# Performance work log

Hardware: AMD Instinct MI355X
Metric: run time of the kernel (lower is better)

The kernel has to match this reference:

```python
import jax, jax.numpy as jnp
import numpy as np

N = 50000
E = 800000
IN_C = 128
HID_C = 128
OUT_C = 128
N_CLS = 40


def setup_inputs() -> dict:
    key = jax.random.key(0)
    ks = jax.random.split(key, 12)
    x = jax.random.normal(ks[0], (N, IN_C), dtype=jnp.float32)
    edge_index = jax.random.randint(ks[1], (2, E), 0, N, dtype=jnp.int64)
    s = 1.0 / np.sqrt(IN_C)
    W_l1 = jax.random.uniform(ks[2], (IN_C, HID_C), jnp.float32, -s, s)
    W_r1 = jax.random.uniform(ks[3], (IN_C, HID_C), jnp.float32, -s, s)
    b1 = jax.random.uniform(ks[4], (HID_C,), jnp.float32, -s, s)
    s2 = 1.0 / np.sqrt(HID_C)
    W_l2 = jax.random.uniform(ks[5], (HID_C, OUT_C), jnp.float32, -s2, s2)
    W_r2 = jax.random.uniform(ks[6], (HID_C, OUT_C), jnp.float32, -s2, s2)
    b2 = jax.random.uniform(ks[7], (OUT_C,), jnp.float32, -s2, s2)
    s3 = 1.0 / np.sqrt(OUT_C)
    W_c = jax.random.uniform(ks[8], (OUT_C, N_CLS), jnp.float32, -s3, s3)
    b_c = jax.random.uniform(ks[9], (N_CLS,), jnp.float32, -s3, s3)
    return {"x": x, "edge_index": edge_index, "W_l1": W_l1, "W_r1": W_r1,
            "b1": b1, "W_l2": W_l2, "W_r2": W_r2, "b2": b2,
            "W_c": W_c, "b_c": b_c}


def _mean_aggregate(x, src, dst, deg_inv):
    # gather source node features over edges, scatter-mean to dst nodes
    msg = x[src]  # [E, C]
    agg = jax.ops.segment_sum(msg, dst, num_segments=N)  # [N, C]
    return agg * deg_inv[:, None]


def _sage_conv(x, src, dst, deg_inv, W_l, W_r, b):
    # PyG SAGEConv (mean aggr): out = agg @ W_l + x @ W_r + b
    agg = _mean_aggregate(x, src, dst, deg_inv)
    return agg @ W_l + x @ W_r + b


def reference(x, edge_index, W_l1, W_r1, b1, W_l2, W_r2, b2, W_c, b_c):
    src, dst = edge_index[0], edge_index[1]
    deg = jax.ops.segment_sum(jnp.ones((E,), jnp.float32), dst, num_segments=N)
    deg_inv = jnp.where(deg > 0, 1.0 / jnp.maximum(deg, 1.0), 0.0)
    h = jax.nn.relu(_sage_conv(x, src, dst, deg_inv, W_l1, W_r1, b1))
    h = jax.nn.relu(_sage_conv(h, src, dst, deg_inv, W_l2, W_r2, b2))
    return h @ W_c + b_c
```

## Files before the change

kernel.cpp:

```cpp
#include <hip/hip_runtime.h>

#define N_NODES 50000
#define N_EDGES 800000
#define C 128
#define NCLS 40
#define KB 98
#define BCAP 9216

typedef short bf16x8 __attribute__((ext_vector_type(8)));
typedef float f32x4 __attribute__((ext_vector_type(4)));
typedef unsigned short ushort_t;

__device__ __forceinline__ unsigned short f32_to_bf16(float f) {
    union { float f; unsigned u; } c; c.f = f;
    unsigned r = (c.u + 0x7FFFu + ((c.u >> 16) & 1u)) >> 16;
    return (unsigned short)r;
}
__device__ __forceinline__ float bf_lo(unsigned u) {
    union { unsigned u; float f; } c; c.u = u << 16; return c.f;
}
__device__ __forceinline__ float bf_hi(unsigned u) {
    union { unsigned u; float f; } c; c.u = u & 0xffff0000u; return c.f;
}
__device__ __forceinline__ unsigned pack_bf16(float lo, float hi) {
    return (unsigned)f32_to_bf16(lo) | ((unsigned)f32_to_bf16(hi) << 16);
}

__global__ __launch_bounds__(256)
void convert_all(const float* __restrict__ Wl1, const float* __restrict__ Wr1,
                 const float* __restrict__ Wl2, const float* __restrict__ Wr2,
                 const float* __restrict__ Wc,  const float* __restrict__ x,
                 ushort_t* __restrict__ Wbf1, ushort_t* __restrict__ Wbf2,
                 ushort_t* __restrict__ Wcb,  ushort_t* __restrict__ xb) {
    int b = blockIdx.x;
    int tid = threadIdx.x;
    if (b < 256) {
        const float* Wl = (b < 128) ? Wl1 : Wl2;
        const float* Wr = (b < 128) ? Wr1 : Wr2;
        ushort_t* Bpre  = (b < 128) ? Wbf1 : Wbf2;
        int idx = (b & 127) * 256 + tid;
        int n = idx >> 8;
        int k = idx & 255;
        float v = (k < 128) ? Wl[k * 128 + n] : Wr[(k - 128) * 128 + n];
        Bpre[n * 256 + k] = f32_to_bf16(v);
    } else if (b < 280) {
        int idx = (b - 256) * 256 + tid;
        if (idx < 48 * 128) {
            int n = idx >> 7;
            int k = idx & 127;
            float v = (n < NCLS) ? Wc[k * NCLS + n] : 0.f;
            Wcb[idx] = f32_to_bf16(v);
        }
    } else {
        int idx = (b - 280) * 256 + tid;
        const float4 v0 = *(const float4*)&x[idx * 8];
        const float4 v1 = *(const float4*)&x[idx * 8 + 4];
        uint4 o;
        o.x = pack_bf16(v0.x, v0.y);
        o.y = pack_bf16(v0.z, v0.w);
        o.z = pack_bf16(v1.x, v1.y);
        o.w = pack_bf16(v1.z, v1.w);
        ((uint4*)xb)[idx] = o;
    }
}

__global__ __launch_bounds__(256)
void bin_kernel(const int* __restrict__ src, const int* __restrict__ dst,
                int* __restrict__ bucket_cnt, unsigned* __restrict__ bucket_data) {
    __shared__ int lh[KB];
    int tid = threadIdx.x;
    int e0 = blockIdx.x * 4096;
    if (tid < KB) lh[tid] = 0;
    __syncthreads();
#pragma unroll
    for (int j = 0; j < 16; ++j) {
        int e = e0 + j * 256 + tid;
        if (e < N_EDGES) atomicAdd(&lh[dst[e] >> 9], 1);
    }
    __syncthreads();
    if (tid < KB) lh[tid] = atomicAdd(&bucket_cnt[tid], lh[tid]);
    __syncthreads();
#pragma unroll
    for (int j = 0; j < 16; ++j) {
        int e = e0 + j * 256 + tid;
        if (e < N_EDGES) {
            int d = dst[e];
            int b = d >> 9;
            int pos = atomicAdd(&lh[b], 1);
            if (pos < BCAP)
                bucket_data[b * BCAP + pos] = (unsigned)src[e] | ((unsigned)(d & 511) << 16);
        }
    }
}

__global__ __launch_bounds__(256)
void build_kernel(const int* __restrict__ bucket_cnt, const unsigned* __restrict__ bucket_data,
                  int* __restrict__ row_ptr, ushort_t* __restrict__ csr16,
                  int* __restrict__ perm) {
    __shared__ int wt[4];
    __shared__ int wt2[4];
    __shared__ int sbases[128];
    __shared__ int hist[512];
    __shared__ int loff[512];
    __shared__ int dhist[64];
    __shared__ ushort_t lcsr[BCAP];
    int tid = threadIdx.x;
    int b = blockIdx.x;
    int n0 = b << 9;
    int nb = min(512, N_NODES - n0);

    int v = 0, x = 0;
    if (tid < 128) {
        v = (tid < KB) ? bucket_cnt[tid] : 0;
        x = v;
#pragma unroll
        for (int off = 1; off < 64; off <<= 1) {
            int t = __shfl_up(x, off, 64);
            if ((tid & 63) >= off) x += t;
        }
        if ((tid & 63) == 63) wt[tid >> 6] = x;
    }
    hist[tid] = 0; hist[tid + 256] = 0;
    __syncthreads();
    if (tid < 128) sbases[tid] = x - v + ((tid >= 64) ? wt[0] : 0);
    __syncthreads();
    int base = sbases[b];
    int ecnt = min(bucket_cnt[b], BCAP);

    for (int i = tid; i < ecnt; i += 256)
        atomicAdd(&hist[bucket_data[b * BCAP + i] >> 16], 1);
    __syncthreads();

    int h0 = hist[2 * tid], h1 = hist[2 * tid + 1];
    int s = h0 + h1;
    int y = s;
#pragma unroll
    for (int off = 1; off < 64; off <<= 1) {
        int t = __shfl_up(y, off, 64);
        if ((tid & 63) >= off) y += t;
    }
    if ((tid & 63) == 63) wt2[tid >> 6] = y;
    __syncthreads();
    int add = 0;
    for (int j = 0; j < (tid >> 6); ++j) add += wt2[j];
    int ex = y + add - s;
    loff[2 * tid] = ex;
    loff[2 * tid + 1] = ex + h0;
    __syncthreads();

    for (int n = tid; n < nb; n += 256) row_ptr[n0 + n] = base + loff[n];
    if (b == KB - 1 && tid == 0) row_ptr[N_NODES] = N_EDGES;
    __syncthreads();

    for (int i = tid; i < ecnt; i += 256) {
        unsigned e = bucket_data[b * BCAP + i];
        int pos = atomicAdd(&loff[e >> 16], 1);
        lcsr[pos] = (ushort_t)(e & 0xFFFFu);
    }
    __syncthreads();
    for (int i = tid; i < ecnt; i += 256) csr16[base + i] = lcsr[i];

    if (tid < 64) dhist[tid] = 0;
    for (int p = tid; p < 512; p += 256) perm[(b << 9) + p] = -1;
    __syncthreads();
    int na = 2 * tid, nbb = 2 * tid + 1;
    int c0 = min(h0, 63), c1 = min(h1, 63);
    if (na < nb)  atomicAdd(&dhist[c0], 1);
    if (nbb < nb) atomicAdd(&dhist[c1], 1);
    __syncthreads();
    if (tid < 64) {
        int v2 = dhist[tid];
        int xs = v2;
#pragma unroll
        for (int off = 1; off < 64; off <<= 1) {
            int t = __shfl_up(xs, off, 64);
            if (tid >= off) xs += t;
        }
        dhist[tid] = xs - v2;
    }
    __syncthreads();
    if (na < nb)  { int pos = atomicAdd(&dhist[c0], 1); perm[(b << 9) + pos] = n0 + na; }
    if (nbb < nb) { int pos = atomicAdd(&dhist[c1], 1); perm[(b << 9) + pos] = n0 + nbb; }
}

__global__ __launch_bounds__(256)
void gather_kernel(const ushort_t* __restrict__ feat,
                   const int* __restrict__ row_ptr,
                   const ushort_t* __restrict__ csr16,
                   const int* __restrict__ perm,
                   ushort_t* __restrict__ agg) {
    const int tid = threadIdx.x;
    const int q = tid & 15;
    const int g = tid >> 4;
    int slot = blockIdx.x * 16 + g;
    int node = perm[slot];
    if (node < 0) return;
    int beg = row_ptr[node], end = row_ptr[node + 1];
    int deg = end - beg;
    const uint4* fb = (const uint4*)feat;

    float a0[8], a1[8], a2[8], a3[8];
#pragma unroll
    for (int j = 0; j < 8; ++j) { a0[j] = 0.f; a1[j] = 0.f; a2[j] = 0.f; a3[j] = 0.f; }

    int nquad = deg >> 2;
    int sx0 = 0, sx1 = 0, sx2 = 0, sx3 = 0;
    if (nquad > 0) {
        sx0 = csr16[beg]; sx1 = csr16[beg + 1]; sx2 = csr16[beg + 2]; sx3 = csr16[beg + 3];
    }
    for (int qd = 0; qd < nquad; ++qd) {
        int s0 = sx0, s1 = sx1, s2 = sx2, s3 = sx3;
        uint4 v0 = fb[s0 * 16 + q];
        uint4 v1 = fb[s1 * 16 + q];
        uint4 v2 = fb[s2 * 16 + q];
        uint4 v3 = fb[s3 * 16 + q];
        if (qd + 1 < nquad) {
            int bs = beg + (qd + 1) * 4;
            sx0 = csr16[bs]; sx1 = csr16[bs + 1]; sx2 = csr16[bs + 2]; sx3 = csr16[bs + 3];
        }
        a0[0] += bf_lo(v0.x); a0[1] += bf_hi(v0.x); a0[2] += bf_lo(v0.y); a0[3] += bf_hi(v0.y);
        a0[4] += bf_lo(v0.z); a0[5] += bf_hi(v0.z); a0[6] += bf_lo(v0.w); a0[7] += bf_hi(v0.w);
        a1[0] += bf_lo(v1.x); a1[1] += bf_hi(v1.x); a1[2] += bf_lo(v1.y); a1[3] += bf_hi(v1.y);
        a1[4] += bf_lo(v1.z); a1[5] += bf_hi(v1.z); a1[6] += bf_lo(v1.w); a1[7] += bf_hi(v1.w);
        a2[0] += bf_lo(v2.x); a2[1] += bf_hi(v2.x); a2[2] += bf_lo(v2.y); a2[3] += bf_hi(v2.y);
        a2[4] += bf_lo(v2.z); a2[5] += bf_hi(v2.z); a2[6] += bf_lo(v2.w); a2[7] += bf_hi(v2.w);
        a3[0] += bf_lo(v3.x); a3[1] += bf_hi(v3.x); a3[2] += bf_lo(v3.y); a3[3] += bf_hi(v3.y);
        a3[4] += bf_lo(v3.z); a3[5] += bf_hi(v3.z); a3[6] += bf_lo(v3.w); a3[7] += bf_hi(v3.w);
    }
    int i0 = beg + nquad * 4;
    int rem = end - i0;
    if (rem > 0) {
        int s0 = csr16[i0];
        int s1 = csr16[i0 + (rem > 1 ? 1 : 0)];
        int s2 = csr16[i0 + (rem > 2 ? 2 : 0)];
        uint4 v0 = fb[s0 * 16 + q];
        uint4 v1 = fb[s1 * 16 + q];
        uint4 v2 = fb[s2 * 16 + q];
        float m1 = rem > 1 ? 1.f : 0.f;
        float m2 = rem > 2 ? 1.f : 0.f;
        a0[0] += bf_lo(v0.x); a0[1] += bf_hi(v0.x); a0[2] += bf_lo(v0.y); a0[3] += bf_hi(v0.y);
        a0[4] += bf_lo(v0.z); a0[5] += bf_hi(v0.z); a0[6] += bf_lo(v0.w); a0[7] += bf_hi(v0.w);
        a1[0] += m1 * bf_lo(v1.x); a1[1] += m1 * bf_hi(v1.x); a1[2] += m1 * bf_lo(v1.y); a1[3] += m1 * bf_hi(v1.y);
        a1[4] += m1 * bf_lo(v1.z); a1[5] += m1 * bf_hi(v1.z); a1[6] += m1 * bf_lo(v1.w); a1[7] += m1 * bf_hi(v1.w);
        a2[0] += m2 * bf_lo(v2.x); a2[1] += m2 * bf_hi(v2.x); a2[2] += m2 * bf_lo(v2.y); a2[3] += m2 * bf_hi(v2.y);
        a2[4] += m2 * bf_lo(v2.z); a2[5] += m2 * bf_hi(v2.z); a2[6] += m2 * bf_lo(v2.w); a2[7] += m2 * bf_hi(v2.w);
    }
    float di = deg > 0 ? 1.f / (float)deg : 0.f;
    float r[8];
#pragma unroll
    for (int j = 0; j < 8; ++j) r[j] = (a0[j] + a1[j] + a2[j] + a3[j]) * di;
    uint4 o;
    o.x = pack_bf16(r[0], r[1]);
    o.y = pack_bf16(r[2], r[3]);
    o.z = pack_bf16(r[4], r[5]);
    o.w = pack_bf16(r[6], r[7]);
    *(uint4*)&agg[node * C + q * 8] = o;
}

#define ALD 136
template<int CLS>
__global__ __launch_bounds__(256)
void gemm_layer(const ushort_t* __restrict__ agg,
                const ushort_t* __restrict__ feat,
                const ushort_t* __restrict__ Bpre,
                const float* __restrict__ bias,
                ushort_t* __restrict__ hout,
                const ushort_t* __restrict__ Wcb,
                const float* __restrict__ bc,
                float* __restrict__ out) {
    __shared__ ushort_t stg[64 * 40 + 128 * 40];
    __shared__ ushort_t h2L[CLS ? 64 * ALD : 4];
    ushort_t* As = stg;
    ushort_t* Bs = stg + 64 * 40;
    const int tid = threadIdx.x;
    const int r0 = blockIdx.x * 64;
    const int w = tid >> 6, lane = tid & 63, m = lane & 15, quad = lane >> 4;

    f32x4 acc[8];
#pragma unroll
    for (int t = 0; t < 8; ++t) acc[t] = (f32x4){0.f, 0.f, 0.f, 0.f};

    for (int kc = 0; kc < 8; ++kc) {
        if (kc) __syncthreads();
        {
            int row = tid >> 2;
            int kq = tid & 3;
            int rg = r0 + row; if (rg >= N_NODES) rg = N_NODES - 1;
            const ushort_t* srcp = (kc < 4) ? agg : feat;
            uint4 v = *(const uint4*)&srcp[rg * C + (kc & 3) * 32 + kq * 8];
            *(uint4*)&As[row * 40 + kq * 8] = v;
        }
#pragma unroll
        for (int i = 0; i < 2; ++i) {
            int slot = tid + i * 256;
            int n = slot >> 2;
            int qq = slot & 3;
            *(uint4*)&Bs[n * 40 + qq * 8] = *(const uint4*)&Bpre[n * 256 + kc * 32 + qq * 8];
        }
        __syncthreads();
        bf16x8 af = *(const bf16x8*)&As[(w * 16 + m) * 40 + quad * 8];
#pragma unroll
        for (int t = 0; t < 8; ++t) {
            bf16x8 bf = *(const bf16x8*)&Bs[(t * 16 + m) * 40 + quad * 8];
            acc[t] = __builtin_amdgcn_mfma_f32_16x16x32_bf16(af, bf, acc[t], 0, 0, 0);
        }
    }

    if (CLS == 0) {
#pragma unroll
        for (int t = 0; t < 8; ++t) {
            int colv = t * 16 + m;
            float bv = bias[colv];
#pragma unroll
            for (int reg = 0; reg < 4; ++reg) {
                int rg = r0 + w * 16 + quad * 4 + reg;
                if (rg < N_NODES) {
                    float vv = fmaxf(acc[t][reg] + bv, 0.f);
                    hout[rg * C + colv] = f32_to_bf16(vv);
                }
            }
        }
    } else {
        __syncthreads();
#pragma unroll
        for (int t = 0; t < 8; ++t) {
            int colv = t * 16 + m;
            float bv = bias[colv];
#pragma unroll
            for (int reg = 0; reg < 4; ++reg) {
                int rl = w * 16 + quad * 4 + reg;
                float vv = fmaxf(acc[t][reg] + bv, 0.f);
                h2L[rl * ALD + colv] = f32_to_bf16(vv);
            }
        }
#pragma unroll
        for (int i = 0; i < 3; ++i) {
            int slot = tid + i * 256;
            int n = slot >> 4, kq = slot & 15;
            uint4 vv = *(const uint4*)&Wcb[n * C + kq * 8];
            *(uint4*)&stg[(kq >> 2) * (48 * 40) + n * 40 + (kq & 3) * 8] = vv;
        }
        __syncthreads();
        f32x4 acc2[3];
#pragma unroll
        for (int t = 0; t < 3; ++t) acc2[t] = (f32x4){0.f, 0.f, 0.f, 0.f};
#pragma unroll
        for (int kc = 0; kc < 4; ++kc) {
            bf16x8 af = *(const bf16x8*)&h2L[(w * 16 + m) * ALD + kc * 32 + quad * 8];
#pragma unroll
            for (int t = 0; t < 3; ++t) {
                bf16x8 bf = *(const bf16x8*)&stg[kc * (48 * 40) + (t * 16 + m) * 40 + quad * 8];
                acc2[t] = __builtin_amdgcn_mfma_f32_16x16x32_bf16(af, bf, acc2[t], 0, 0, 0);
            }
        }
#pragma unroll
        for (int t = 0; t < 3; ++t) {
            int col = t * 16 + m;
            if (col < NCLS) {
                float bvv = bc[col];
#pragma unroll
                for (int reg = 0; reg < 4; ++reg) {
                    int rg = r0 + w * 16 + quad * 4 + reg;
                    if (rg < N_NODES) out[rg * NCLS + col] = acc2[t][reg] + bvv;
                }
            }
        }
    }
}

extern "C" void kernel_launch(void* const* d_in, const int* in_sizes, int n_in,
                              void* d_out, int out_size, void* d_ws, size_t ws_size,
                              hipStream_t stream) {
    const float* x   = (const float*)d_in[0];
    const int*   ei  = (const int*)d_in[1];
    const float* Wl1 = (const float*)d_in[2];
    const float* Wr1 = (const float*)d_in[3];
    const float* b1  = (const float*)d_in[4];
    const float* Wl2 = (const float*)d_in[5];
    const float* Wr2 = (const float*)d_in[6];
    const float* b2  = (const float*)d_in[7];
    const float* Wc  = (const float*)d_in[8];
    const float* bc  = (const float*)d_in[9];
    const int* srcI = ei;
    const int* dstI = ei + N_EDGES;
    float* out = (float*)d_out;

    ushort_t* xb   = (ushort_t*)d_ws;
    ushort_t* h1b  = xb + (size_t)N_NODES * C;
    ushort_t* Wbf1 = h1b + (size_t)N_NODES * C;
    ushort_t* Wbf2 = Wbf1 + 32768;
    ushort_t* Wcb  = Wbf2 + 32768;
    ushort_t* csr16 = Wcb + 6144;
    int* bucket_cnt = (int*)(csr16 + N_EDGES);
    int* row_ptr    = bucket_cnt + 128;
    unsigned* bucket_data = (unsigned*)(row_ptr + N_NODES + 1);
    int* perm = (int*)(bucket_data + (size_t)KB * BCAP);
    ushort_t* aggb = (ushort_t*)(perm + KB * 512);

    convert_all<<<280 + (N_NODES * C / 8 + 255) / 256, 256, 0, stream>>>(
        Wl1, Wr1, Wl2, Wr2, Wc, x, Wbf1, Wbf2, Wcb, xb);

    hipMemsetAsync(bucket_cnt, 0, 128 * sizeof(int), stream);
    bin_kernel<<<(N_EDGES + 4095) / 4096, 256, 0, stream>>>(srcI, dstI, bucket_cnt, bucket_data);
    build_kernel<<<KB, 256, 0, stream>>>(bucket_cnt, bucket_data, row_ptr, csr16, perm);

    gather_kernel<<<KB * 512 / 16, 256, 0, stream>>>(xb, row_ptr, csr16, perm, aggb);
    gemm_layer<0><<<(N_NODES + 63) / 64, 256, 0, stream>>>(
        aggb, xb, Wbf1, b1, h1b, nullptr, nullptr, nullptr);

    gather_kernel<<<KB * 512 / 16, 256, 0, stream>>>(h1b, row_ptr, csr16, perm, aggb);
    gemm_layer<1><<<(N_NODES + 63) / 64, 256, 0, stream>>>(
        aggb, h1b, Wbf2, b2, nullptr, Wcb, bc, out);
}
```

Measured before the change: 224.0 us.

## Stage full weight matrix in LDS once and widen gather unroll to eight edges

The GEMM kernel now loads the whole 128x256 bf16 weight block into LDS once (padded stride 264) and reads the A fragments straight from global into registers. This replaces the eight-step K loop that restaged tiles and synchronised twice per step. The aggregation kernel issues eight feature gathers per iteration instead of four, with a four-edge and masked tail, to put more memory requests in flight. The cost is more LDS per block (about 66KB), which may cut occupancy, plus more registers in the gather loop.

```diff
diff --git a/kernel.cpp b/kernel.cpp
--- a/kernel.cpp
+++ b/kernel.cpp
@@ -6,6 +6,7 @@
 #define NCLS 40
 #define KB 98
 #define BCAP 9216
+#define WLD 264
 
 typedef short bf16x8 __attribute__((ext_vector_type(8)));
 typedef float f32x4 __attribute__((ext_vector_type(4)));
@@ -24,6 +25,17 @@
 }
 __device__ __forceinline__ unsigned pack_bf16(float lo, float hi) {
     return (unsigned)f32_to_bf16(lo) | ((unsigned)f32_to_bf16(hi) << 16);
+}
+__device__ __forceinline__ bf16x8 as_bf(uint4 u) {
+    union { uint4 u; bf16x8 b; } c; c.u = u; return c.b;
+}
+__device__ __forceinline__ void acc8(float* a, uint4 v) {
+    a[0] += bf_lo(v.x); a[1] += bf_hi(v.x); a[2] += bf_lo(v.y); a[3] += bf_hi(v.y);
+    a[4] += bf_lo(v.z); a[5] += bf_hi(v.z); a[6] += bf_lo(v.w); a[7] += bf_hi(v.w);
+}
+__device__ __forceinline__ void acc8m(float* a, uint4 v, float mk) {
+    a[0] += mk * bf_lo(v.x); a[1] += mk * bf_hi(v.x); a[2] += mk * bf_lo(v.y); a[3] += mk * bf_hi(v.y);
+    a[4] += mk * bf_lo(v.z); a[5] += mk * bf_hi(v.z); a[6] += mk * bf_lo(v.w); a[7] += mk * bf_hi(v.w);
 }
 
 __global__ __launch_bounds__(256)
@@ -203,47 +215,50 @@
 #pragma unroll
     for (int j = 0; j < 8; ++j) { a0[j] = 0.f; a1[j] = 0.f; a2[j] = 0.f; a3[j] = 0.f; }
 
-    int nquad = deg >> 2;
-    int sx0 = 0, sx1 = 0, sx2 = 0, sx3 = 0;
-    if (nquad > 0) {
-        sx0 = csr16[beg]; sx1 = csr16[beg + 1]; sx2 = csr16[beg + 2]; sx3 = csr16[beg + 3];
-    }
-    for (int qd = 0; qd < nquad; ++qd) {
-        int s0 = sx0, s1 = sx1, s2 = sx2, s3 = sx3;
+    int n8 = deg >> 3;
+    int s0 = 0, s1 = 0, s2 = 0, s3 = 0, s4 = 0, s5 = 0, s6 = 0, s7 = 0;
+    if (n8 > 0) {
+        s0 = csr16[beg];     s1 = csr16[beg + 1]; s2 = csr16[beg + 2]; s3 = csr16[beg + 3];
+        s4 = csr16[beg + 4]; s5 = csr16[beg + 5]; s6 = csr16[beg + 6]; s7 = csr16[beg + 7];
+    }
+    for (int it = 0; it < n8; ++it) {
         uint4 v0 = fb[s0 * 16 + q];
         uint4 v1 = fb[s1 * 16 + q];
         uint4 v2 = fb[s2 * 16 + q];
         uint4 v3 = fb[s3 * 16 + q];
-        if (qd + 1 < nquad) {
-            int bs = beg + (qd + 1) * 4;
-            sx0 = csr16[bs]; sx1 = csr16[bs + 1]; sx2 = csr16[bs + 2]; sx3 = csr16[bs + 3];
-        }
-        a0[0] += bf_lo(v0.x); a0[1] += bf_hi(v0.x); a0[2] += bf_lo(v0.y); a0[3] += bf_hi(v0.y);
-        a0[4] += bf_lo(v0.z); a0[5] += bf_hi(v0.z); a0[6] += bf_lo(v0.w); a0[7] += bf_hi(v0.w);
-        a1[0] += bf_lo(v1.x); a1[1] += bf_hi(v1.x); a1[2] += bf_lo(v1.y); a1[3] += bf_hi(v1.y);
-        a1[4] += bf_lo(v1.z); a1[5] += bf_hi(v1.z); a1[6] += bf_lo(v1.w); a1[7] += bf_hi(v1.w);
-        a2[0] += bf_lo(v2.x); a2[1] += bf_hi(v2.x); a2[2] += bf_lo(v2.y); a2[3] += bf_hi(v2.y);
-        a2[4] += bf_lo(v2.z); a2[5] += bf_hi(v2.z); a2[6] += bf_lo(v2.w); a2[7] += bf_hi(v2.w);
-        a3[0] += bf_lo(v3.x); a3[1] += bf_hi(v3.x); a3[2] += bf_lo(v3.y); a3[3] += bf_hi(v3.y);
-        a3[4] += bf_lo(v3.z); a3[5] += bf_hi(v3.z); a3[6] += bf_lo(v3.w); a3[7] += bf_hi(v3.w);
-    }
-    int i0 = beg + nquad * 4;
-    int rem = end - i0;
+        uint4 v4 = fb[s4 * 16 + q];
+        uint4 v5 = fb[s5 * 16 + q];
+        uint4 v6 = fb[s6 * 16 + q];
+        uint4 v7 = fb[s7 * 16 + q];
+        if (it + 1 < n8) {
+            int bs = beg + (it + 1) * 8;
+            s0 = csr16[bs];     s1 = csr16[bs + 1]; s2 = csr16[bs + 2]; s3 = csr16[bs + 3];
+            s4 = csr16[bs + 4]; s5 = csr16[bs + 5]; s6 = csr16[bs + 6]; s7 = csr16[bs + 7];
+        }
+        acc8(a0, v0); acc8(a1, v1); acc8(a2, v2); acc8(a3, v3);
+        acc8(a0, v4); acc8(a1, v5); acc8(a2, v6); acc8(a3, v7);
+    }
+    int i = beg + n8 * 8;
+    if (i + 4 <= end) {
+        int t0 = csr16[i], t1 = csr16[i + 1], t2 = csr16[i + 2], t3 = csr16[i + 3];
+        uint4 v0 = fb[t0 * 16 + q];
+        uint4 v1 = fb[t1 * 16 + q];
+        uint4 v2 = fb[t2 * 16 + q];
+        uint4 v3 = fb[t3 * 16 + q];
+        acc8(a0, v0); acc8(a1, v1); acc8(a2, v2); acc8(a3, v3);
+        i += 4;
+    }
+    int rem = end - i;
     if (rem > 0) {
-        int s0 = csr16[i0];
-        int s1 = csr16[i0 + (rem > 1 ? 1 : 0)];
-        int s2 = csr16[i0 + (rem > 2 ? 2 : 0)];
-        uint4 v0 = fb[s0 * 16 + q];
-        uint4 v1 = fb[s1 * 16 + q];
-        uint4 v2 = fb[s2 * 16 + q];
-        float m1 = rem > 1 ? 1.f : 0.f;
-        float m2 = rem > 2 ? 1.f : 0.f;
-        a0[0] += bf_lo(v0.x); a0[1] += bf_hi(v0.x); a0[2] += bf_lo(v0.y); a0[3] += bf_hi(v0.y);
-        a0[4] += bf_lo(v0.z); a0[5] += bf_hi(v0.z); a0[6] += bf_lo(v0.w); a0[7] += bf_hi(v0.w);
-        a1[0] += m1 * bf_lo(v1.x); a1[1] += m1 * bf_hi(v1.x); a1[2] += m1 * bf_lo(v1.y); a1[3] += m1 * bf_hi(v1.y);
-        a1[4] += m1 * bf_lo(v1.z); a1[5] += m1 * bf_hi(v1.z); a1[6] += m1 * bf_lo(v1.w); a1[7] += m1 * bf_hi(v1.w);
-        a2[0] += m2 * bf_lo(v2.x); a2[1] += m2 * bf_hi(v2.x); a2[2] += m2 * bf_lo(v2.y); a2[3] += m2 * bf_hi(v2.y);
-        a2[4] += m2 * bf_lo(v2.z); a2[5] += m2 * bf_hi(v2.z); a2[6] += m2 * bf_lo(v2.w); a2[7] += m2 * bf_hi(v2.w);
+        int t0 = csr16[i];
+        int t1 = csr16[i + (rem > 1 ? 1 : 0)];
+        int t2 = csr16[i + (rem > 2 ? 2 : 0)];
+        uint4 v0 = fb[t0 * 16 + q];
+        uint4 v1 = fb[t1 * 16 + q];
+        uint4 v2 = fb[t2 * 16 + q];
+        acc8(a0, v0);
+        acc8m(a1, v1, rem > 1 ? 1.f : 0.f);
+        acc8m(a2, v2, rem > 2 ? 1.f : 0.f);
     }
     float di = deg > 0 ? 1.f / (float)deg : 0.f;
     float r[8];
@@ -257,7 +272,7 @@
     *(uint4*)&agg[node * C + q * 8] = o;
 }
 
-#define ALD 136
+#define HLD 136
 template<int CLS>
 __global__ __launch_bounds__(256)
 void gemm_layer(const ushort_t* __restrict__ agg,
@@ -268,40 +283,37 @@
                 const ushort_t* __restrict__ Wcb,
                 const float* __restrict__ bc,
                 float* __restrict__ out) {
-    __shared__ ushort_t stg[64 * 40 + 128 * 40];
-    __shared__ ushort_t h2L[CLS ? 64 * ALD : 4];
-    ushort_t* As = stg;
-    ushort_t* Bs = stg + 64 * 40;
+    __shared__ ushort_t Wlds[128 * WLD];
     const int tid = threadIdx.x;
     const int r0 = blockIdx.x * 64;
     const int w = tid >> 6, lane = tid & 63, m = lane & 15, quad = lane >> 4;
 
+#pragma unroll
+    for (int i = 0; i < 16; ++i) {
+        int idx = i * 256 + tid;
+        int row = idx >> 5, c32 = idx & 31;
+        *(uint4*)&Wlds[row * WLD + c32 * 8] = *(const uint4*)&Bpre[row * 256 + c32 * 8];
+    }
+
+    int rg = r0 + w * 16 + m; if (rg >= N_NODES) rg = N_NODES - 1;
+    uint4 afa[4], aff[4];
+#pragma unroll
+    for (int kc = 0; kc < 4; ++kc) afa[kc] = *(const uint4*)&agg[rg * C + kc * 32 + quad * 8];
+#pragma unroll
+    for (int kc = 0; kc < 4; ++kc) aff[kc] = *(const uint4*)&feat[rg * C + kc * 32 + quad * 8];
+
+    __syncthreads();
+
     f32x4 acc[8];
 #pragma unroll
     for (int t = 0; t < 8; ++t) acc[t] = (f32x4){0.f, 0.f, 0.f, 0.f};
 
+#pragma unroll
     for (int kc = 0; kc < 8; ++kc) {
-        if (kc) __syncthreads();
-        {
-            int row = tid >> 2;
-            int kq = tid & 3;
-            int rg = r0 + row; if (rg >= N_NODES) rg = N_NODES - 1;
-            const ushort_t* srcp = (kc < 4) ? agg : feat;
-            uint4 v = *(const uint4*)&srcp[rg * C + (kc & 3) * 32 + kq * 8];
-            *(uint4*)&As[row * 40 + kq * 8] = v;
-        }
-#pragma unroll
-        for (int i = 0; i < 2; ++i) {
-            int slot = tid + i * 256;
-            int n = slot >> 2;
-            int qq = slot & 3;
-            *(uint4*)&Bs[n * 40 + qq * 8] = *(const uint4*)&Bpre[n * 256 + kc * 32 + qq * 8];
-        }
-        __syncthreads();
-        bf16x8 af = *(const bf16x8*)&As[(w * 16 + m) * 40 + quad * 8];
+        bf16x8 af = (kc < 4) ? as_bf(afa[kc]) : as_bf(aff[kc - 4]);
 #pragma unroll
         for (int t = 0; t < 8; ++t) {
-            bf16x8 bf = *(const bf16x8*)&Bs[(t * 16 + m) * 40 + quad * 8];
+            bf16x8 bf = *(const bf16x8*)&Wlds[(t * 16 + m) * WLD + kc * 32 + quad * 8];
             acc[t] = __builtin_amdgcn_mfma_f32_16x16x32_bf16(af, bf, acc[t], 0, 0, 0);
         }
     }
@@ -313,14 +325,16 @@
             float bv = bias[colv];
 #pragma unroll
             for (int reg = 0; reg < 4; ++reg) {
-                int rg = r0 + w * 16 + quad * 4 + reg;
-                if (rg < N_NODES) {
+                int rs = r0 + w * 16 + quad * 4 + reg;
+                if (rs < N_NODES) {
                     float vv = fmaxf(acc[t][reg] + bv, 0.f);
-                    hout[rg * C + colv] = f32_to_bf16(vv);
+                    hout[rs * C + colv] = f32_to_bf16(vv);
                 }
             }
         }
     } else {
+        ushort_t* h2L = Wlds;
+        ushort_t* WcL = Wlds + 64 * HLD;
         __syncthreads();
 #pragma unroll
         for (int t = 0; t < 8; ++t) {
@@ -330,15 +344,14 @@
             for (int reg = 0; reg < 4; ++reg) {
                 int rl = w * 16 + quad * 4 + reg;
                 float vv = fmaxf(acc[t][reg] + bv, 0.f);
-                h2L[rl * ALD + colv] = f32_to_bf16(vv);
+                h2L[rl * HLD + colv] = f32_to_bf16(vv);
             }
         }
 #pragma unroll
         for (int i = 0; i < 3; ++i) {
             int slot = tid + i * 256;
-            int n = slot >> 4, kq = slot & 15;
-            uint4 vv = *(const uint4*)&Wcb[n * C + kq * 8];
-            *(uint4*)&stg[(kq >> 2) * (48 * 40) + n * 40 + (kq & 3) * 8] = vv;
+            int n = slot >> 4, c16 = slot & 15;
+            *(uint4*)&WcL[n * HLD + c16 * 8] = *(const uint4*)&Wcb[n * C + c16 * 8];
         }
         __syncthreads();
         f32x4 acc2[3];
@@ -346,10 +359,10 @@
         for (int t = 0; t < 3; ++t) acc2[t] = (f32x4){0.f, 0.f, 0.f, 0.f};
 #pragma unroll
         for (int kc = 0; kc < 4; ++kc) {
-            bf16x8 af = *(const bf16x8*)&h2L[(w * 16 + m) * ALD + kc * 32 + quad * 8];
+            bf16x8 af = *(const bf16x8*)&h2L[(w * 16 + m) * HLD + kc * 32 + quad * 8];
 #pragma unroll
             for (int t = 0; t < 3; ++t) {
-                bf16x8 bf = *(const bf16x8*)&stg[kc * (48 * 40) + (t * 16 + m) * 40 + quad * 8];
+                bf16x8 bf = *(const bf16x8*)&WcL[(t * 16 + m) * HLD + kc * 32 + quad * 8];
                 acc2[t] = __builtin_amdgcn_mfma_f32_16x16x32_bf16(af, bf, acc2[t], 0, 0, 0);
             }
         }
@@ -360,8 +373,8 @@
                 float bvv = bc[col];
 #pragma unroll
                 for (int reg = 0; reg < 4; ++reg) {
-                    int rg = r0 + w * 16 + quad * 4 + reg;
-                    if (rg < N_NODES) out[rg * NCLS + col] = acc2[t][reg] + bvv;
+                    int rs = r0 + w * 16 + quad * 4 + reg;
+                    if (rs < N_NODES) out[rs * NCLS + col] = acc2[t][reg] + bvv;
                 }
             }
         }
```

After: 222.1 us. About the same (-0.8%).
